# Optimization experiments

Measured on AMD Instinct MI355X. Metric: run time of the kernel, lower is better.

## Reference

```python
import jax, jax.numpy as jnp
import numpy as np

TRIANGLE_TABLE = np.array([
    [-1, -1, -1, -1, -1, -1], [1, 0, 2, -1, -1, -1], [4, 0, 3, -1, -1, -1], [1, 4, 2, 1, 3, 4],
    [3, 1, 5, -1, -1, -1], [2, 3, 0, 2, 5, 3], [1, 4, 0, 1, 5, 4], [4, 2, 5, -1, -1, -1],
    [4, 5, 2, -1, -1, -1], [4, 1, 0, 4, 5, 1], [3, 2, 0, 3, 5, 2], [1, 3, 5, -1, -1, -1],
    [4, 1, 2, 4, 3, 1], [3, 0, 4, -1, -1, -1], [2, 0, 1, -1, -1, -1], [-1, -1, -1, -1, -1, -1]], np.int32)
NUM_TRIANGLES_TABLE = np.array([0, 1, 1, 2, 1, 2, 2, 1, 1, 2, 2, 1, 2, 1, 1, 0], np.int32)
BASE_TET_EDGES = np.array([0, 1, 0, 2, 0, 3, 1, 2, 1, 3, 2, 3], np.int32)


def _make_tet_grid(R):
    # Regular grid in [0,1]^3, each cube split into 6 tets along the 0-7 diagonal.
    r1 = R + 1
    gi, gj, gk = np.meshgrid(np.arange(r1), np.arange(r1), np.arange(r1), indexing='ij')
    verts = (np.stack([gi, gj, gk], -1).reshape(-1, 3) / R).astype(np.float32)  # (Nv,3)
    ci, cj, ck = np.meshgrid(np.arange(R), np.arange(R), np.arange(R), indexing='ij')
    ci, cj, ck = ci.ravel(), cj.ravel(), ck.ravel()
    def vid(dx, dy, dz):
        return ((ci + dx) * r1 + (cj + dy)) * r1 + (ck + dz)
    corners = [vid((c >> 2) & 1, (c >> 1) & 1, c & 1) for c in range(8)]
    tet_corners = [(0, 1, 3, 7), (0, 3, 2, 7), (0, 2, 6, 7), (0, 6, 4, 7), (0, 4, 5, 7), (0, 5, 1, 7)]
    tets = np.stack([np.stack([corners[a] for a in t], -1) for t in tet_corners], 1).reshape(-1, 4)
    return verts, tets.astype(np.int32)


def setup_inputs() -> dict:
    R = 64
    verts, tets = _make_tet_grid(R)
    key = jax.random.key(0)
    k1, k2 = jax.random.split(key)
    level = jax.random.normal(k1, (verts.shape[0],), dtype=jnp.float32)
    deformation = jax.random.normal(k2, (verts.shape[0], 3), dtype=jnp.float32)
    return {
        'level': level,
        'deformation': deformation,
        'grid_vertices': jnp.asarray(verts),
        'tet_indices': jnp.asarray(tets),
        'resolution': R,
    }


def reference(level, deformation, grid_vertices, tet_indices, resolution):
    # normalize_grid_deformation: (range_hi - range_lo)/res * tanh(offsets), range = (0,1)
    pos = grid_vertices + jnp.tanh(deformation) / resolution  # (Nv,3)
    occ = level > 0                                           # (Nv,)
    occ_f = occ[tet_indices]                                  # (F,4)
    occ_sum = occ_f.sum(-1)
    valid = (occ_sum > 0) & (occ_sum < 4)
    vt = tet_indices[valid]                                   # (Fv,4)
    occ_valid = occ_f[valid]                                  # (Fv,4)
    # per-tet edges, each sorted (min,max) -> dedup
    edges = vt[:, jnp.asarray(BASE_TET_EDGES)].reshape(-1, 2)  # (6*Fv,2)
    edges = jnp.sort(edges, axis=1)
    unique_edges, idx_map = jnp.unique(edges, axis=0, return_inverse=True)
    idx_map = idx_map.reshape(-1)
    # edges that actually cross the isosurface (exactly one endpoint inside)
    mask_edges = occ[unique_edges].sum(-1) == 1               # (U,)
    mapping = jnp.where(mask_edges, jnp.cumsum(mask_edges.astype(jnp.int32)) - 1, -1)
    idx_map = mapping[idx_map].reshape(-1, 6)                 # (Fv,6)
    interp_v = unique_edges[mask_edges]                       # (M,2)
    # linear interpolation of crossing point along each edge
    ep = pos[interp_v]                                        # (M,2,3)
    es = level[interp_v] * jnp.array([1.0, -1.0], dtype=level.dtype)  # (M,2) = [sdf0, -sdf1]
    w = es[:, ::-1] / es.sum(1, keepdims=True)                # (M,2) = [-sdf1, sdf0]/(sdf0-sdf1)
    verts_out = (ep * w[:, :, None]).sum(1)                   # (M,3)
    # triangle table lookup
    v_id = jnp.array([1, 2, 4, 8], dtype=jnp.int32)
    tetindex = (occ_valid.astype(jnp.int32) * v_id).sum(-1)   # (Fv,)
    tri_tab = jnp.asarray(TRIANGLE_TABLE)
    num_tri = jnp.asarray(NUM_TRIANGLES_TABLE)[tetindex]
    m1 = num_tri == 1
    m2 = num_tri == 2
    f1 = jnp.take_along_axis(idx_map[m1], tri_tab[tetindex[m1]][:, :3], axis=1).reshape(-1, 3)
    f2 = jnp.take_along_axis(idx_map[m2], tri_tab[tetindex[m2]][:, :6], axis=1).reshape(-1, 3)
    faces = jnp.concatenate([f1, f2], axis=0)                 # (Nf,3)
    return verts_out, faces
```

## Files before the change

kernel.cpp:

```cpp
#include <hip/hip_runtime.h>
#include <math.h>


typedef unsigned long long ull;

#define ST_LD(p)    __hip_atomic_load((p), __ATOMIC_RELAXED, __HIP_MEMORY_SCOPE_AGENT)
#define ST_ST(p,v)  __hip_atomic_store((p), (v), __ATOMIC_RELAXED, __HIP_MEMORY_SCOPE_AGENT)

__device__ __forceinline__ float fast_tanh(float x) {
    float e = __expf(2.0f * x);
    return __fdividef(e - 1.0f, e + 1.0f);
}

__device__ __constant__ int c_tri_tab[16][6] = {
    {-1,-1,-1,-1,-1,-1},{1,0,2,-1,-1,-1},{4,0,3,-1,-1,-1},{1,4,2,1,3,4},
    {3,1,5,-1,-1,-1},{2,3,0,2,5,3},{1,4,0,1,5,4},{4,2,5,-1,-1,-1},
    {4,5,2,-1,-1,-1},{4,1,0,4,5,1},{3,2,0,3,5,2},{1,3,5,-1,-1,-1},
    {4,1,2,4,3,1},{3,0,4,-1,-1,-1},{2,0,1,-1,-1,-1},{-1,-1,-1,-1,-1,-1}};
__device__ __constant__ int c_num_tri[16] = {0,1,1,2,1,2,2,1,1,2,2,1,2,1,1,0};
__device__ __constant__ int c_tc[6][4] = {{0,1,3,7},{0,3,2,7},{0,2,6,7},{0,6,4,7},{0,4,5,7},{0,5,1,7}};
__device__ __constant__ int c_te[6][6] = {
    {(0<<3)|0,(0<<3)|2,(0<<3)|6,(1<<3)|1,(1<<3)|5,(3<<3)|3},
    {(0<<3)|2,(0<<3)|1,(0<<3)|6,(2<<3)|0,(3<<3)|3,(2<<3)|4},
    {(0<<3)|1,(0<<3)|5,(0<<3)|6,(2<<3)|3,(2<<3)|4,(6<<3)|0},
    {(0<<3)|5,(0<<3)|3,(0<<3)|6,(4<<3)|1,(6<<3)|0,(4<<3)|2},
    {(0<<3)|3,(0<<3)|4,(0<<3)|6,(4<<3)|0,(4<<3)|2,(5<<3)|1},
    {(0<<3)|4,(0<<3)|0,(0<<3)|6,(1<<3)|3,(5<<3)|1,(1<<3)|5}};

#define TAG      (1ull << 62)
#define PMASK    ((1ull << 60) - 1ull)
#define READY(s) (((s) >> 62) == 1ull)

__global__ void k_vert(const float* __restrict__ level, const float* __restrict__ deform,
                       int NV, int r1, float invR,
                       ull* __restrict__ stateA, ull* __restrict__ prefS,
                       unsigned* __restrict__ rankWord, unsigned char* __restrict__ obByte,
                       uint2* __restrict__ cubeRank, int* __restrict__ totals,
                       float* __restrict__ out) {
    int b = blockIdx.x;
    int v = b * 256 + threadIdx.x;
    int R = r1 - 1, rsq = r1 * r1;
    bool valid = v < NV;
    float la = valid ? level[v] : 0.f;
    bool occv = valid && (la > 0.f);

    int x = 0, y = 0, z = 0, flags = 0, n1 = 0, n2 = 0, cidx = 0;
    bool interior = false;
    float lb[7];
    if (valid) {
        x = v / rsq; int rem = v - x * rsq; y = rem / r1; z = rem - y * r1;
        bool bx = x < R, by = y < R, bz = z < R;
        interior = bx && by && bz;
        bool inb[7] = {bz, by, by && bz, bx, bx && bz, bx && by, interior};
        int deltas[7] = {1, r1, r1 + 1, rsq, rsq + 1, rsq + r1, rsq + r1 + 1};
        int ob = occv ? 1 : 0;
        for (int j = 0; j < 7; j++) {
            float l = inb[j] ? level[v + deltas[j]] : 0.f;
            lb[j] = l;
            bool o = inb[j] && (l > 0.f);
            ob |= (o ? 1 : 0) << (j + 1);
            if (inb[j] && (o != occv)) flags |= 1 << j;
        }
        if (interior) {
            cidx = ((x * R) + y) * R + z;
            obByte[cidx] = (unsigned char)ob;
            for (int k = 0; k < 6; k++) {
                int ti = ((ob >> c_tc[k][0]) & 1) | (((ob >> c_tc[k][1]) & 1) << 1)
                       | (((ob >> c_tc[k][2]) & 1) << 2) | (((ob >> c_tc[k][3]) & 1) << 3);
                int n = c_num_tri[ti];
                n1 += (n == 1); n2 += (n == 2);
            }
        }
    }
    int cnt = __popc(flags);
    int pk = n1 | (n2 << 16);
    int lane = threadIdx.x & 63, wv = threadIdx.x >> 6;
    int inclE = cnt, inclT = pk;
    for (int o = 1; o < 64; o <<= 1) {
        int tE = __shfl_up(inclE, o);
        int tT = __shfl_up(inclT, o);
        if (lane >= o) { inclE += tE; inclT += tT; }
    }
    __shared__ int wE[4], wT[4];
    __shared__ ull sExcl;
    if (lane == 63) { wE[wv] = inclE; wT[wv] = inclT; }
    __syncthreads();

    if (wv == 0) {
        int eb = 0, t1b = 0, t2b = 0;
        if (lane == 0) {
            eb = wE[0] + wE[1] + wE[2] + wE[3];
            int tb = wT[0] + wT[1] + wT[2] + wT[3];
            t1b = tb & 0xffff; t2b = tb >> 16;
            ST_ST(&stateA[b], TAG | ((ull)eb << 40) | ((ull)t1b << 20) | (ull)t2b);
        }
        ull sum = 0;
        for (int w = 0; 64 * w < b; w++) {
            int i = b - 1 - 64 * w - lane;
            ull pv = (i >= 0) ? ST_LD(&prefS[i]) : 0;
            ull pm = __ballot(i >= 0 && READY(pv));
            int Lp = pm ? (__ffsll((long long)pm) - 1) : 64;
            ull val = 0;
            if (i >= 0 && lane < Lp) {
                ull s;
                do { s = ST_LD(&stateA[i]); } while (!READY(s));
                val = s & PMASK;
            } else if (i >= 0 && lane == Lp) {
                val = pv & PMASK;
            }
            for (int o = 1; o < 64; o <<= 1) val += __shfl_xor(val, o);
            sum += val;
            if (Lp < 64) break;
        }
        if (lane == 0) {
            sExcl = sum;
            ull inc = sum + (((ull)eb << 40) | ((ull)t1b << 20) | (ull)t2b);
            ST_ST(&prefS[b], TAG | inc);
            if (b == (int)gridDim.x - 1) {
                totals[0] = (int)((inc >> 40) & 0xFFFFF);
                totals[1] = (int)((inc >> 20) & 0xFFFFF);
                totals[2] = (int)(inc & 0xFFFFF);
            }
        }
    }
    __syncthreads();

    ull ex = sExcl;
    int exclE = (int)((ex >> 40) & 0xFFFFF);
    int excl1 = (int)((ex >> 20) & 0xFFFFF);
    int excl2 = (int)(ex & 0xFFFFF);
    int woffE = 0, woffT = 0;
    for (int w = 0; w < wv; w++) { woffE += wE[w]; woffT += wT[w]; }
    int rank0 = exclE + woffE + inclE - cnt;
    int tExcl = woffT + inclT - pk;
    if (interior)
        cubeRank[cidx] = make_uint2((unsigned)(excl1 + (tExcl & 0xffff)),
                                    (unsigned)(excl2 + (tExcl >> 16)));

    if (valid)
        rankWord[v] = (unsigned)rank0 | ((unsigned)flags << 21);

    if (flags) {
        int deltas[7] = {1, r1, r1 + 1, rsq, rsq + 1, rsq + r1, rsq + r1 + 1};
        const int dxs[7] = {0, 0, 0, 1, 1, 1, 1};
        const int dys[7] = {0, 1, 1, 0, 0, 1, 1};
        const int dzs[7] = {1, 0, 1, 0, 1, 0, 1};
        float pax = x * invR + fast_tanh(deform[3 * v])     * invR;
        float pay = y * invR + fast_tanh(deform[3 * v + 1]) * invR;
        float paz = z * invR + fast_tanh(deform[3 * v + 2]) * invR;
        int r = rank0;
        for (int j = 0; j < 7; j++) {
            if (!((flags >> j) & 1)) continue;
            int bb = v + deltas[j];
            float lbv = lb[j];
            float inv = __fdividef(1.0f, la - lbv);
            float w0 = -lbv * inv;
            float w1f = la * inv;
            float pbx = (x + dxs[j]) * invR + fast_tanh(deform[3 * bb])     * invR;
            float pby = (y + dys[j]) * invR + fast_tanh(deform[3 * bb + 1]) * invR;
            float pbz = (z + dzs[j]) * invR + fast_tanh(deform[3 * bb + 2]) * invR;
            out[3 * r]     = pax * w0 + pbx * w1f;
            out[3 * r + 1] = pay * w0 + pby * w1f;
            out[3 * r + 2] = paz * w0 + pbz * w1f;
            r++;
        }
    }
}

__global__ void k_face(int NV, int r1, int NT,
                       const unsigned char* __restrict__ obByte,
                       const uint2* __restrict__ cubeRank,
                       const unsigned* __restrict__ rankWord, const int* __restrict__ totals,
                       float* __restrict__ out) {
    __shared__ ull tab[256];
    if (threadIdx.x < 256) {
        int ob = threadIdx.x;
        ull w = 0;
        for (int k = 0; k < 6; k++) {
            int ti = ((ob >> c_tc[k][0]) & 1) | (((ob >> c_tc[k][1]) & 1) << 1)
                   | (((ob >> c_tc[k][2]) & 1) << 2) | (((ob >> c_tc[k][3]) & 1) << 3);
            w |= (ull)ti << (4 * k);
            w |= (ull)c_num_tri[ti] << (32 + 2 * k);
        }
        tab[ob] = w;
    }
    __syncthreads();

    int t = blockIdx.x * 256 + threadIdx.x;
    if (t >= NT) return;
    int c = t / 6;
    int k = t - c * 6;
    int ob = obByte[c];
    ull w = tab[ob];
    int nt = (int)(w >> (32 + 2 * k)) & 3;
    if (nt == 0) return;
    int ti = (int)(w >> (4 * k)) & 15;
    int pre1 = 0, pre2 = 0;
    for (int kk = 0; kk < k; kk++) {
        int m = (int)(w >> (32 + 2 * kk)) & 3;
        pre1 += (m == 1); pre2 += (m == 2);
    }
    uint2 cr = cubeRank[c];
    int R = r1 - 1, rsq = r1 * r1;
    int rr = R * R;
    int cx = c / rr; int rem = c - cx * rr; int cy = rem / R; int cz = rem - cy * R;
    int v = (cx * r1 + cy) * r1 + cz;

    int M = totals[0], N1 = totals[1];
    float* faces = out + 3 * (size_t)M;
    int off[8] = {0, 1, r1, r1 + 1, rsq, rsq + 1, rsq + r1, rsq + r1 + 1};
    int ne = nt * 3;
    float vals[6];
    for (int e = 0; e < ne; e++) {
        int le = c_tri_tab[ti][e];
        int ce = c_te[k][le];
        int a = v + off[ce >> 3];
        int j = ce & 7;
        unsigned rw = rankWord[a];
        int rk = (int)(rw & 0x1FFFFF) + __popc((rw >> 21) & (unsigned)((1 << j) - 1));
        vals[e] = (float)rk;
    }
    if (nt == 1) {
        size_t base = 3 * (size_t)(cr.x + pre1);
        faces[base] = vals[0]; faces[base + 1] = vals[1]; faces[base + 2] = vals[2];
    } else {
        size_t base = 3 * ((size_t)N1 + 2 * (size_t)(cr.y + pre2));
        for (int e = 0; e < 6; e++) faces[base + e] = vals[e];
    }
}

extern "C" void kernel_launch(void* const* d_in, const int* in_sizes, int n_in,
                              void* d_out, int out_size, void* d_ws, size_t ws_size,
                              hipStream_t stream) {
    const float* level  = (const float*)d_in[0];
    const float* deform = (const float*)d_in[1];
    int NV = in_sizes[0];
    int r1 = 1;
    while ((long long)r1 * r1 * r1 < (long long)NV) r1++;
    int R = r1 - 1;
    float invR = 1.0f / (float)R;

    int nb = (NV + 255) / 256;
    int NC = R * R * R;
    int NT = 6 * NC;
    int nbT = (NT + 255) / 256;

    char* w = (char*)d_ws;
    unsigned* rankWord = (unsigned*)w;
    w += (((size_t)NV * sizeof(unsigned)) + 255) & ~(size_t)255;
    unsigned char* obByte = (unsigned char*)w;
    w += (((size_t)NC) + 255) & ~(size_t)255;
    uint2* cubeRank = (uint2*)w;
    w += (((size_t)NC * 8) + 255) & ~(size_t)255;
    ull* stateA = (ull*)w;
    ull* prefS = stateA + nb;
    int* totals = (int*)(prefS + nb);

    float* out = (float*)d_out;

    k_vert<<<nb, 256, 0, stream>>>(level, deform, NV, r1, invR, stateA, prefS,
                                   rankWord, obByte, cubeRank, totals, out);
    k_face<<<nbT, 256, 0, stream>>>(NV, r1, NT, obByte, cubeRank, rankWord, totals, out);
}
```

Before: 130.1 us.

## Replace decoupled look-back scan with separate count kernel and per-block reduction

```diff
diff --git a/kernel.cpp b/kernel.cpp
--- a/kernel.cpp
+++ b/kernel.cpp
@@ -3,9 +3,6 @@
 
 
 typedef unsigned long long ull;
-
-#define ST_LD(p)    __hip_atomic_load((p), __ATOMIC_RELAXED, __HIP_MEMORY_SCOPE_AGENT)
-#define ST_ST(p,v)  __hip_atomic_store((p), (v), __ATOMIC_RELAXED, __HIP_MEMORY_SCOPE_AGENT)
 
 __device__ __forceinline__ float fast_tanh(float x) {
     float e = __expf(2.0f * x);
@@ -27,54 +24,72 @@
     {(0<<3)|3,(0<<3)|4,(0<<3)|6,(4<<3)|0,(4<<3)|2,(5<<3)|1},
     {(0<<3)|4,(0<<3)|0,(0<<3)|6,(1<<3)|3,(5<<3)|1,(1<<3)|5}};
 
-#define TAG      (1ull << 62)
-#define PMASK    ((1ull << 60) - 1ull)
-#define READY(s) (((s) >> 62) == 1ull)
+__device__ __forceinline__ void phase_a(const float* __restrict__ level, int v, int NV,
+                                        int r1, int& flags, int& pk, int& ob,
+                                        bool& interior, float (&lb)[7], float& la) {
+    int R = r1 - 1, rsq = r1 * r1;
+    flags = 0; pk = 0; ob = 0; interior = false; la = 0.f;
+    if (v >= NV) return;
+    la = level[v];
+    bool occv = la > 0.f;
+    int x = v / rsq; int rem = v - x * rsq; int y = rem / r1; int z = rem - y * r1;
+    bool bx = x < R, by = y < R, bz = z < R;
+    interior = bx && by && bz;
+    bool inb[7] = {bz, by, by && bz, bx, bx && bz, bx && by, interior};
+    int deltas[7] = {1, r1, r1 + 1, rsq, rsq + 1, rsq + r1, rsq + r1 + 1};
+    ob = occv ? 1 : 0;
+    for (int j = 0; j < 7; j++) {
+        float l = inb[j] ? level[v + deltas[j]] : 0.f;
+        lb[j] = l;
+        bool o = inb[j] && (l > 0.f);
+        ob |= (o ? 1 : 0) << (j + 1);
+        if (inb[j] && (o != occv)) flags |= 1 << j;
+    }
+    if (interior) {
+        int n1 = 0, n2 = 0;
+        for (int k = 0; k < 6; k++) {
+            int ti = ((ob >> c_tc[k][0]) & 1) | (((ob >> c_tc[k][1]) & 1) << 1)
+                   | (((ob >> c_tc[k][2]) & 1) << 2) | (((ob >> c_tc[k][3]) & 1) << 3);
+            int n = c_num_tri[ti];
+            n1 += (n == 1); n2 += (n == 2);
+        }
+        pk = n1 | (n2 << 16);
+    }
+}
+
+__global__ void k_count(const float* __restrict__ level, int NV, int r1,
+                        ull* __restrict__ stateA) {
+    int v = blockIdx.x * 256 + threadIdx.x;
+    int flags, pk, ob; bool interior; float lb[7], la;
+    phase_a(level, v, NV, r1, flags, pk, ob, interior, lb, la);
+    int eS = __popc(flags), tS = pk;
+    for (int o = 1; o < 64; o <<= 1) { eS += __shfl_xor(eS, o); tS += __shfl_xor(tS, o); }
+    __shared__ int wE[4], wT[4];
+    int lane = threadIdx.x & 63, wv = threadIdx.x >> 6;
+    if (lane == 0) { wE[wv] = eS; wT[wv] = tS; }
+    __syncthreads();
+    if (threadIdx.x == 0) {
+        int eb = wE[0] + wE[1] + wE[2] + wE[3];
+        int tb = wT[0] + wT[1] + wT[2] + wT[3];
+        stateA[blockIdx.x] = ((ull)eb << 40) | ((ull)(tb & 0xffff) << 20) | (ull)(tb >> 16);
+    }
+}
 
 __global__ void k_vert(const float* __restrict__ level, const float* __restrict__ deform,
-                       int NV, int r1, float invR,
-                       ull* __restrict__ stateA, ull* __restrict__ prefS,
+                       int NV, int r1, float invR, int nb,
+                       const ull* __restrict__ stateA,
                        unsigned* __restrict__ rankWord, unsigned char* __restrict__ obByte,
                        uint2* __restrict__ cubeRank, int* __restrict__ totals,
                        float* __restrict__ out) {
     int b = blockIdx.x;
     int v = b * 256 + threadIdx.x;
     int R = r1 - 1, rsq = r1 * r1;
-    bool valid = v < NV;
-    float la = valid ? level[v] : 0.f;
-    bool occv = valid && (la > 0.f);
-
-    int x = 0, y = 0, z = 0, flags = 0, n1 = 0, n2 = 0, cidx = 0;
-    bool interior = false;
-    float lb[7];
-    if (valid) {
-        x = v / rsq; int rem = v - x * rsq; y = rem / r1; z = rem - y * r1;
-        bool bx = x < R, by = y < R, bz = z < R;
-        interior = bx && by && bz;
-        bool inb[7] = {bz, by, by && bz, bx, bx && bz, bx && by, interior};
-        int deltas[7] = {1, r1, r1 + 1, rsq, rsq + 1, rsq + r1, rsq + r1 + 1};
-        int ob = occv ? 1 : 0;
-        for (int j = 0; j < 7; j++) {
-            float l = inb[j] ? level[v + deltas[j]] : 0.f;
-            lb[j] = l;
-            bool o = inb[j] && (l > 0.f);
-            ob |= (o ? 1 : 0) << (j + 1);
-            if (inb[j] && (o != occv)) flags |= 1 << j;
-        }
-        if (interior) {
-            cidx = ((x * R) + y) * R + z;
-            obByte[cidx] = (unsigned char)ob;
-            for (int k = 0; k < 6; k++) {
-                int ti = ((ob >> c_tc[k][0]) & 1) | (((ob >> c_tc[k][1]) & 1) << 1)
-                       | (((ob >> c_tc[k][2]) & 1) << 2) | (((ob >> c_tc[k][3]) & 1) << 3);
-                int n = c_num_tri[ti];
-                n1 += (n == 1); n2 += (n == 2);
-            }
-        }
-    }
+    int lane = threadIdx.x & 63, wv = threadIdx.x >> 6;
+
+    int flags, pk, ob; bool interior; float lb[7], la;
+    phase_a(level, v, NV, r1, flags, pk, ob, interior, lb, la);
     int cnt = __popc(flags);
-    int pk = n1 | (n2 << 16);
-    int lane = threadIdx.x & 63, wv = threadIdx.x >> 6;
+
     int inclE = cnt, inclT = pk;
     for (int o = 1; o < 64; o <<= 1) {
         int tE = __shfl_up(inclE, o);
@@ -82,87 +97,68 @@
         if (lane >= o) { inclE += tE; inclT += tT; }
     }
     __shared__ int wE[4], wT[4];
-    __shared__ ull sExcl;
+    __shared__ ull sEx[4], sAll[4];
     if (lane == 63) { wE[wv] = inclE; wT[wv] = inclT; }
+
+    ull sB = 0, sA = 0;
+    for (int i = threadIdx.x; i < nb; i += 256) {
+        ull s = stateA[i];
+        sA += s;
+        if (i < b) sB += s;
+    }
+    for (int o = 1; o < 64; o <<= 1) { sB += __shfl_xor(sB, o); sA += __shfl_xor(sA, o); }
+    if (lane == 0) { sEx[wv] = sB; sAll[wv] = sA; }
     __syncthreads();
-
-    if (wv == 0) {
-        int eb = 0, t1b = 0, t2b = 0;
-        if (lane == 0) {
-            eb = wE[0] + wE[1] + wE[2] + wE[3];
-            int tb = wT[0] + wT[1] + wT[2] + wT[3];
-            t1b = tb & 0xffff; t2b = tb >> 16;
-            ST_ST(&stateA[b], TAG | ((ull)eb << 40) | ((ull)t1b << 20) | (ull)t2b);
-        }
-        ull sum = 0;
-        for (int w = 0; 64 * w < b; w++) {
-            int i = b - 1 - 64 * w - lane;
-            ull pv = (i >= 0) ? ST_LD(&prefS[i]) : 0;
-            ull pm = __ballot(i >= 0 && READY(pv));
-            int Lp = pm ? (__ffsll((long long)pm) - 1) : 64;
-            ull val = 0;
-            if (i >= 0 && lane < Lp) {
-                ull s;
-                do { s = ST_LD(&stateA[i]); } while (!READY(s));
-                val = s & PMASK;
-            } else if (i >= 0 && lane == Lp) {
-                val = pv & PMASK;
-            }
-            for (int o = 1; o < 64; o <<= 1) val += __shfl_xor(val, o);
-            sum += val;
-            if (Lp < 64) break;
-        }
-        if (lane == 0) {
-            sExcl = sum;
-            ull inc = sum + (((ull)eb << 40) | ((ull)t1b << 20) | (ull)t2b);
-            ST_ST(&prefS[b], TAG | inc);
-            if (b == (int)gridDim.x - 1) {
-                totals[0] = (int)((inc >> 40) & 0xFFFFF);
-                totals[1] = (int)((inc >> 20) & 0xFFFFF);
-                totals[2] = (int)(inc & 0xFFFFF);
-            }
-        }
-    }
-    __syncthreads();
-
-    ull ex = sExcl;
-    int exclE = (int)((ex >> 40) & 0xFFFFF);
-    int excl1 = (int)((ex >> 20) & 0xFFFFF);
-    int excl2 = (int)(ex & 0xFFFFF);
+    ull exP  = sEx[0] + sEx[1] + sEx[2] + sEx[3];
+    ull allP = sAll[0] + sAll[1] + sAll[2] + sAll[3];
+    int exclE = (int)((exP >> 40) & 0xFFFFF);
+    int excl1 = (int)((exP >> 20) & 0xFFFFF);
+    int excl2 = (int)(exP & 0xFFFFF);
+    if (b == 0 && threadIdx.x == 0) {
+        totals[0] = (int)((allP >> 40) & 0xFFFFF);
+        totals[1] = (int)((allP >> 20) & 0xFFFFF);
+        totals[2] = (int)(allP & 0xFFFFF);
+    }
+
     int woffE = 0, woffT = 0;
     for (int w = 0; w < wv; w++) { woffE += wE[w]; woffT += wT[w]; }
     int rank0 = exclE + woffE + inclE - cnt;
     int tExcl = woffT + inclT - pk;
-    if (interior)
-        cubeRank[cidx] = make_uint2((unsigned)(excl1 + (tExcl & 0xffff)),
-                                    (unsigned)(excl2 + (tExcl >> 16)));
-
-    if (valid)
+
+    if (v < NV) {
+        int x = v / rsq; int rem = v - x * rsq; int y = rem / r1; int z = rem - y * r1;
+        if (interior) {
+            int cidx = ((x * R) + y) * R + z;
+            obByte[cidx] = (unsigned char)ob;
+            cubeRank[cidx] = make_uint2((unsigned)(excl1 + (tExcl & 0xffff)),
+                                        (unsigned)(excl2 + (tExcl >> 16)));
+        }
         rankWord[v] = (unsigned)rank0 | ((unsigned)flags << 21);
 
-    if (flags) {
-        int deltas[7] = {1, r1, r1 + 1, rsq, rsq + 1, rsq + r1, rsq + r1 + 1};
-        const int dxs[7] = {0, 0, 0, 1, 1, 1, 1};
-        const int dys[7] = {0, 1, 1, 0, 0, 1, 1};
-        const int dzs[7] = {1, 0, 1, 0, 1, 0, 1};
-        float pax = x * invR + fast_tanh(deform[3 * v])     * invR;
-        float pay = y * invR + fast_tanh(deform[3 * v + 1]) * invR;
-        float paz = z * invR + fast_tanh(deform[3 * v + 2]) * invR;
-        int r = rank0;
-        for (int j = 0; j < 7; j++) {
-            if (!((flags >> j) & 1)) continue;
-            int bb = v + deltas[j];
-            float lbv = lb[j];
-            float inv = __fdividef(1.0f, la - lbv);
-            float w0 = -lbv * inv;
-            float w1f = la * inv;
-            float pbx = (x + dxs[j]) * invR + fast_tanh(deform[3 * bb])     * invR;
-            float pby = (y + dys[j]) * invR + fast_tanh(deform[3 * bb + 1]) * invR;
-            float pbz = (z + dzs[j]) * invR + fast_tanh(deform[3 * bb + 2]) * invR;
-            out[3 * r]     = pax * w0 + pbx * w1f;
-            out[3 * r + 1] = pay * w0 + pby * w1f;
-            out[3 * r + 2] = paz * w0 + pbz * w1f;
-            r++;
+        if (flags) {
+            int deltas[7] = {1, r1, r1 + 1, rsq, rsq + 1, rsq + r1, rsq + r1 + 1};
+            const int dxs[7] = {0, 0, 0, 1, 1, 1, 1};
+            const int dys[7] = {0, 1, 1, 0, 0, 1, 1};
+            const int dzs[7] = {1, 0, 1, 0, 1, 0, 1};
+            float pax = x * invR + fast_tanh(deform[3 * v])     * invR;
+            float pay = y * invR + fast_tanh(deform[3 * v + 1]) * invR;
+            float paz = z * invR + fast_tanh(deform[3 * v + 2]) * invR;
+            int r = rank0;
+            for (int j = 0; j < 7; j++) {
+                if (!((flags >> j) & 1)) continue;
+                int bb = v + deltas[j];
+                float lbv = lb[j];
+                float inv = __fdividef(1.0f, la - lbv);
+                float w0 = -lbv * inv;
+                float w1f = la * inv;
+                float pbx = (x + dxs[j]) * invR + fast_tanh(deform[3 * bb])     * invR;
+                float pby = (y + dys[j]) * invR + fast_tanh(deform[3 * bb + 1]) * invR;
+                float pbz = (z + dzs[j]) * invR + fast_tanh(deform[3 * bb + 2]) * invR;
+                out[3 * r]     = pax * w0 + pbx * w1f;
+                out[3 * r + 1] = pay * w0 + pby * w1f;
+                out[3 * r + 2] = paz * w0 + pbz * w1f;
+                r++;
+            }
         }
     }
 }
@@ -253,12 +249,12 @@
     uint2* cubeRank = (uint2*)w;
     w += (((size_t)NC * 8) + 255) & ~(size_t)255;
     ull* stateA = (ull*)w;
-    ull* prefS = stateA + nb;
-    int* totals = (int*)(prefS + nb);
+    int* totals = (int*)(stateA + nb);
 
     float* out = (float*)d_out;
 
-    k_vert<<<nb, 256, 0, stream>>>(level, deform, NV, r1, invR, stateA, prefS,
+    k_count<<<nb, 256, 0, stream>>>(level, NV, r1, stateA);
+    k_vert<<<nb, 256, 0, stream>>>(level, deform, NV, r1, invR, nb, stateA,
                                    rankWord, obByte, cubeRank, totals, out);
     k_face<<<nbT, 256, 0, stream>>>(NV, r1, NT, obByte, cubeRank, rankWord, totals, out);
 }
```

Result: no change. 130.8 us (+0.5%).
